# Performance work log

Measured on AMD Instinct MI355X. Metric: run time of the kernel, lower is better.

The kernel has to match this reference:

```python
import jax, jax.numpy as jnp
import numpy as np

N_TX, N_ACC, E = 500000, 100000, 1000000
D_TX, D_ACC, H = 64, 32, 64


def setup_inputs() -> dict:
    key = jax.random.key(0)
    ks = jax.random.split(key, 16)
    s = 0.05
    return {
        "x_tx": jax.random.normal(ks[0], (N_TX, D_TX), jnp.float32),
        "x_acc": jax.random.normal(ks[1], (N_ACC, D_ACC), jnp.float32),
        "pays_src": jax.random.randint(ks[2], (E,), 0, N_ACC),
        "pays_dst": jax.random.randint(ks[3], (E,), 0, N_TX),
        "rev_src": jax.random.randint(ks[4], (E,), 0, N_TX),
        "rev_dst": jax.random.randint(ks[5], (E,), 0, N_ACC),
        # SAGEConv for ('account','pays','transaction'): lin_l: D_ACC->H (bias), lin_r: D_TX->H (no bias)
        "Wl_pays": jax.random.normal(ks[6], (D_ACC, H), jnp.float32) * s,
        "bl_pays": jnp.zeros((H,), jnp.float32),
        "Wr_pays": jax.random.normal(ks[7], (D_TX, H), jnp.float32) * s,
        # SAGEConv for ('transaction','rev_pays','account'): lin_l: D_TX->H, lin_r: D_ACC->H
        "Wl_rev": jax.random.normal(ks[8], (D_TX, H), jnp.float32) * s,
        "bl_rev": jnp.zeros((H,), jnp.float32),
        "Wr_rev": jax.random.normal(ks[9], (D_ACC, H), jnp.float32) * s,
        # output head Linear(H, 1)
        "W_out": jax.random.normal(ks[10], (H, 1), jnp.float32) * s,
        "b_out": jnp.zeros((1,), jnp.float32),
    }


def _segment_mean(msg, dst, n_dst):
    # scatter-mean: sum per dst node / clamped degree (isolated nodes -> 0)
    s = jax.ops.segment_sum(msg, dst, num_segments=n_dst)
    c = jax.ops.segment_sum(jnp.ones((dst.shape[0], 1), msg.dtype), dst, num_segments=n_dst)
    return s / jnp.maximum(c, 1.0)


def _sage(x_src, x_dst, src, dst, Wl, bl, Wr):
    agg = _segment_mean(x_src[src], dst, x_dst.shape[0])  # [n_dst, d_src]
    return agg @ Wl + bl + x_dst @ Wr  # [n_dst, H]


def reference(x_tx, x_acc, pays_src, pays_dst, rev_src, rev_dst,
              Wl_pays, bl_pays, Wr_pays, Wl_rev, bl_rev, Wr_rev, W_out, b_out):
    # HeteroConv: each dst node type receives exactly one edge type here, so aggr='mean' is identity
    h_tx = _sage(x_acc, x_tx, pays_src, pays_dst, Wl_pays, bl_pays, Wr_pays)
    h_acc = _sage(x_tx, x_acc, rev_src, rev_dst, Wl_rev, bl_rev, Wr_rev)
    tx_x = jax.nn.relu(h_tx)
    _ = jax.nn.relu(h_acc)  # computed by the module but unused downstream
    logits = (tx_x @ W_out + b_out)[:, 0]
    return logits, tx_x
```

## Files before the change

### kernel.cpp

```cpp
#include <hip/hip_runtime.h>

#define N_TX   500000
#define N_ACC  100000
#define E_CNT  1000000
#define D_TX   64
#define D_ACC  32
#define H_DIM  64

#define SCAN_B    256
#define SCAN_I    8
#define SCAN_TILE (SCAN_B * SCAN_I)
#define NSCAN_BLOCKS ((N_TX + SCAN_TILE - 1) / SCAN_TILE)


__global__ __launch_bounds__(256) void hist_kernel(
    const int* __restrict__ dst, int* __restrict__ cnt) {
    int e = blockIdx.x * blockDim.x + threadIdx.x;
    if (e < E_CNT) atomicAdd(&cnt[dst[e]], 1);
}

__global__ __launch_bounds__(SCAN_B) void scan1_kernel(
    const int* __restrict__ cnt, int* __restrict__ offs, int* __restrict__ bsum) {
    __shared__ int lds[SCAN_B];
    int base = blockIdx.x * SCAN_TILE + threadIdx.x * SCAN_I;
    int v[SCAN_I];
    int tsum = 0;
#pragma unroll
    for (int i = 0; i < SCAN_I; ++i) {
        int idx = base + i;
        v[i] = (idx < N_TX) ? cnt[idx] : 0;
        tsum += v[i];
    }
    lds[threadIdx.x] = tsum;
    __syncthreads();
    for (int off = 1; off < SCAN_B; off <<= 1) {
        int a = 0;
        if ((int)threadIdx.x >= off) a = lds[threadIdx.x - off];
        __syncthreads();
        lds[threadIdx.x] += a;
        __syncthreads();
    }
    int texcl = lds[threadIdx.x] - tsum;
    if (threadIdx.x == SCAN_B - 1) bsum[blockIdx.x] = lds[SCAN_B - 1];
    int run = texcl;
#pragma unroll
    for (int i = 0; i < SCAN_I; ++i) {
        int idx = base + i;
        if (idx < N_TX) offs[idx] = run;
        run += v[i];
    }
}

__global__ __launch_bounds__(256) void scan2_kernel(int* __restrict__ bsum, int nb) {
    __shared__ int lds[256];
    int t = threadIdx.x;
    int v = (t < nb) ? bsum[t] : 0;
    lds[t] = v;
    __syncthreads();
    for (int off = 1; off < 256; off <<= 1) {
        int a = 0;
        if (t >= off) a = lds[t - off];
        __syncthreads();
        lds[t] += a;
        __syncthreads();
    }
    if (t < nb) bsum[t] = lds[t] - v;
}

__global__ __launch_bounds__(256) void finalize_kernel(
    int* __restrict__ offs, int* __restrict__ cursors, const int* __restrict__ bsum) {
    int i = blockIdx.x * blockDim.x + threadIdx.x;
    if (i < N_TX) {
        int f = offs[i] + bsum[i / SCAN_TILE];
        offs[i] = f;
        cursors[i] = f;
    }
}

__global__ __launch_bounds__(256) void fill_kernel(
    const int* __restrict__ src, const int* __restrict__ dst,
    int* __restrict__ cursors, int* __restrict__ eidx) {
    int e = blockIdx.x * blockDim.x + threadIdx.x;
    if (e < E_CNT) {
        int d = dst[e];
        int p = atomicAdd(&cursors[d], 1);
        eidx[p] = src[e];
    }
}

__global__ __launch_bounds__(256, 4) void acc_transform_kernel(
    const float* __restrict__ x_acc, const float* __restrict__ Wl,
    float* __restrict__ y, int rows_per_wave) {
    int lane = threadIdx.x & 63;
    int wave = (blockIdx.x * blockDim.x + threadIdx.x) >> 6;
    float wl[D_ACC];
#pragma unroll
    for (int k = 0; k < D_ACC; ++k) wl[k] = Wl[k * H_DIM + lane];
#pragma unroll
    for (int k = 0; k < D_ACC; ++k) asm volatile("" : "+v"(wl[k]));
    int r0 = wave * rows_per_wave;
    int r1 = min(r0 + rows_per_wave, N_ACC);
    for (int row = r0; row < r1; ++row) {
        int urow = __builtin_amdgcn_readfirstlane(row);
        const float4* xr = (const float4*)(x_acc + (size_t)urow * D_ACC);
        float a0 = 0.f, a1 = 0.f, a2 = 0.f, a3 = 0.f;
#pragma unroll
        for (int q = 0; q < 8; ++q) {
            float4 v = xr[q];
            a0 = fmaf(v.x, wl[4 * q + 0], a0);
            a1 = fmaf(v.y, wl[4 * q + 1], a1);
            a2 = fmaf(v.z, wl[4 * q + 2], a2);
            a3 = fmaf(v.w, wl[4 * q + 3], a3);
        }
        y[(size_t)urow * H_DIM + lane] = (a0 + a1) + (a2 + a3);
    }
}

__global__ __launch_bounds__(256, 4) void row_kernel(
    const float* __restrict__ x_tx,
    const float* __restrict__ y,
    const int*   __restrict__ offs,
    const int*   __restrict__ cnt,
    const int*   __restrict__ eidx,
    const float* __restrict__ Wr,
    const float* __restrict__ bl,
    const float* __restrict__ Wout,
    const float* __restrict__ bout,
    float*       __restrict__ logits,
    float*       __restrict__ txx) {
    int lane = threadIdx.x & 63;
    int wave = (blockIdx.x * blockDim.x + threadIdx.x) >> 6;

    int rbase = wave * 64;
    if (rbase >= N_TX) return;
    int nrows = min(64, N_TX - rbase);

    float wr[D_TX];
#pragma unroll
    for (int k = 0; k < D_TX; ++k) wr[k] = Wr[k * H_DIM + lane];
#pragma unroll
    for (int k = 0; k < D_TX; ++k) asm volatile("" : "+v"(wr[k]));
    float b  = bl[lane];
    float wo = Wout[lane];
    float bo = bout[0];
    asm volatile("" : "+v"(b), "+v"(wo), "+v"(bo));

    int deg_l = 0, off_l = 0;
    if (lane < nrows) {
        deg_l = cnt[rbase + lane];
        off_l = offs[rbase + lane];
    }
    int s0_l = 0, s1_l = 0, s2_l = 0, s3_l = 0;
    if (deg_l > 0) s0_l = eidx[off_l];
    if (deg_l > 1) s1_l = eidx[off_l + 1];
    if (deg_l > 2) s2_l = eidx[off_l + 2];
    if (deg_l > 3) s3_l = eidx[off_l + 3];

    int ubase = __builtin_amdgcn_readfirstlane(rbase);

    for (int k = 0; k < nrows; ++k) {
        int urow = ubase + k;
        int deg = __builtin_amdgcn_readlane(deg_l, k);
        int off = __builtin_amdgcn_readlane(off_l, k);
        int s0  = __builtin_amdgcn_readlane(s0_l, k);
        int s1  = __builtin_amdgcn_readlane(s1_l, k);
        int s2  = __builtin_amdgcn_readlane(s2_l, k);
        int s3  = __builtin_amdgcn_readlane(s3_l, k);

        float v0 = 0.f, v1 = 0.f, v2 = 0.f, v3 = 0.f;
        if (deg > 0) v0 = y[(size_t)s0 * H_DIM + lane];
        if (deg > 1) v1 = y[(size_t)s1 * H_DIM + lane];
        if (deg > 2) v2 = y[(size_t)s2 * H_DIM + lane];
        if (deg > 3) v3 = y[(size_t)s3 * H_DIM + lane];

        const float4* xr = (const float4*)(x_tx + (size_t)urow * D_TX);
        float a0 = 0.f, a1 = 0.f, a2 = 0.f, a3 = 0.f;
#pragma unroll
        for (int q = 0; q < 16; ++q) {
            float4 xv = xr[q];
            a0 = fmaf(xv.x, wr[4 * q + 0], a0);
            a1 = fmaf(xv.y, wr[4 * q + 1], a1);
            a2 = fmaf(xv.z, wr[4 * q + 2], a2);
            a3 = fmaf(xv.w, wr[4 * q + 3], a3);
        }

        float g = (v0 + v1) + (v2 + v3);
        for (int e = 4; e < deg; ++e) {
            int se = __builtin_amdgcn_readfirstlane(eidx[off + e]);
            g += y[(size_t)se * H_DIM + lane];
        }

        float inv = 1.0f / (float)(deg > 0 ? deg : 1);
        float h = ((a0 + a1) + (a2 + a3)) + b + g * inv;
        float r = fmaxf(h, 0.f);
        txx[(size_t)urow * H_DIM + lane] = r;

        float p = r * wo;
#pragma unroll
        for (int sh = 32; sh > 0; sh >>= 1) p += __shfl_down(p, sh);
        if (lane == 0) logits[urow] = p + bo;
    }
}

extern "C" void kernel_launch(void* const* d_in, const int* in_sizes, int n_in,
                              void* d_out, int out_size, void* d_ws, size_t ws_size,
                              hipStream_t stream) {
    const float* x_tx     = (const float*)d_in[0];
    const float* x_acc    = (const float*)d_in[1];
    const int*   pays_src = (const int*)d_in[2];
    const int*   pays_dst = (const int*)d_in[3];
    const float* Wl   = (const float*)d_in[6];
    const float* bl   = (const float*)d_in[7];
    const float* Wr   = (const float*)d_in[8];
    const float* Wout = (const float*)d_in[12];
    const float* bout = (const float*)d_in[13];

    float* out    = (float*)d_out;
    float* logits = out;
    float* txx    = out + N_TX;

    int* cnt     = (int*)d_ws;
    int* offs    = cnt + N_TX;
    int* cursors = offs + N_TX;
    int* bsum    = cursors + N_TX;
    int* eidx    = bsum + 1024;
    float* y     = (float*)(eidx + E_CNT);

    hipMemsetAsync(cnt, 0, (size_t)N_TX * sizeof(int), stream);

    hist_kernel<<<(E_CNT + 255) / 256, 256, 0, stream>>>(pays_dst, cnt);
    scan1_kernel<<<NSCAN_BLOCKS, SCAN_B, 0, stream>>>(cnt, offs, bsum);
    scan2_kernel<<<1, 256, 0, stream>>>(bsum, NSCAN_BLOCKS);
    finalize_kernel<<<(N_TX + 255) / 256, 256, 0, stream>>>(offs, cursors, bsum);
    fill_kernel<<<(E_CNT + 255) / 256, 256, 0, stream>>>(pays_src, pays_dst, cursors, eidx);

    {
        const int blocks = 2048;
        int rpw = (N_ACC + blocks * 4 - 1) / (blocks * 4);
        acc_transform_kernel<<<blocks, 256, 0, stream>>>(x_acc, Wl, y, rpw);
    }

    {
        const int waves  = (N_TX + 63) / 64;
        const int blocks = (waves + 3) / 4;
        row_kernel<<<blocks, 256, 0, stream>>>(
            x_tx, y, offs, cnt, eidx, Wr, bl, Wout, bout, logits, txx);
    }
}
```

Baseline: 628.2 us.

## Stage x_tx rows through double-buffered LDS with coalesced register prefetch

The row kernel now loads 16-row tiles of x_tx with coalesced float4 loads across the wave into registers, then stores them into a per-wave double-buffered LDS region. The next tile's global loads are issued before the current tile is computed, overlapping memory latency with the FMA work. The old code used wave-uniform scalar-address loads of each row straight from global memory. In exchange the kernel uses 32KB of LDS per block and more registers, which may lower occupancy. It also adds LDS read traffic in the inner loop.

```diff
diff --git a/kernel.cpp b/kernel.cpp
--- a/kernel.cpp
+++ b/kernel.cpp
@@ -11,6 +11,9 @@
 #define SCAN_I    8
 #define SCAN_TILE (SCAN_B * SCAN_I)
 #define NSCAN_BLOCKS ((N_TX + SCAN_TILE - 1) / SCAN_TILE)
+
+#define TROWS 16
+#define TFL4  (TROWS * H_DIM / 4)
 
 
 __global__ __launch_bounds__(256) void hist_kernel(
@@ -128,12 +131,18 @@
     const float* __restrict__ bout,
     float*       __restrict__ logits,
     float*       __restrict__ txx) {
+    __shared__ float xs[4 * 2 * TROWS * H_DIM];
+
     int lane = threadIdx.x & 63;
+    int wib  = threadIdx.x >> 6;
     int wave = (blockIdx.x * blockDim.x + threadIdx.x) >> 6;
 
     int rbase = wave * 64;
     if (rbase >= N_TX) return;
     int nrows = min(64, N_TX - rbase);
+
+    float* xbuf0 = xs + wib * (2 * TROWS * H_DIM);
+    float* xbuf1 = xbuf0 + TROWS * H_DIM;
 
     float wr[D_TX];
 #pragma unroll
@@ -157,48 +166,87 @@
     if (deg_l > 3) s3_l = eidx[off_l + 3];
 
     int ubase = __builtin_amdgcn_readfirstlane(rbase);
-
-    for (int k = 0; k < nrows; ++k) {
-        int urow = ubase + k;
-        int deg = __builtin_amdgcn_readlane(deg_l, k);
-        int off = __builtin_amdgcn_readlane(off_l, k);
-        int s0  = __builtin_amdgcn_readlane(s0_l, k);
-        int s1  = __builtin_amdgcn_readlane(s1_l, k);
-        int s2  = __builtin_amdgcn_readlane(s2_l, k);
-        int s3  = __builtin_amdgcn_readlane(s3_l, k);
-
-        float v0 = 0.f, v1 = 0.f, v2 = 0.f, v3 = 0.f;
-        if (deg > 0) v0 = y[(size_t)s0 * H_DIM + lane];
-        if (deg > 1) v1 = y[(size_t)s1 * H_DIM + lane];
-        if (deg > 2) v2 = y[(size_t)s2 * H_DIM + lane];
-        if (deg > 3) v3 = y[(size_t)s3 * H_DIM + lane];
-
-        const float4* xr = (const float4*)(x_tx + (size_t)urow * D_TX);
-        float a0 = 0.f, a1 = 0.f, a2 = 0.f, a3 = 0.f;
-#pragma unroll
-        for (int q = 0; q < 16; ++q) {
-            float4 xv = xr[q];
-            a0 = fmaf(xv.x, wr[4 * q + 0], a0);
-            a1 = fmaf(xv.y, wr[4 * q + 1], a1);
-            a2 = fmaf(xv.z, wr[4 * q + 2], a2);
-            a3 = fmaf(xv.w, wr[4 * q + 3], a3);
-        }
-
-        float g = (v0 + v1) + (v2 + v3);
-        for (int e = 4; e < deg; ++e) {
-            int se = __builtin_amdgcn_readfirstlane(eidx[off + e]);
-            g += y[(size_t)se * H_DIM + lane];
-        }
-
-        float inv = 1.0f / (float)(deg > 0 ? deg : 1);
-        float h = ((a0 + a1) + (a2 + a3)) + b + g * inv;
-        float r = fmaxf(h, 0.f);
-        txx[(size_t)urow * H_DIM + lane] = r;
-
-        float p = r * wo;
-#pragma unroll
-        for (int sh = 32; sh > 0; sh >>= 1) p += __shfl_down(p, sh);
-        if (lane == 0) logits[urow] = p + bo;
+    const float4* xsrc = (const float4*)(x_tx + (size_t)ubase * D_TX);
+
+    float4 st[4];
+#pragma unroll
+    for (int j = 0; j < 4; ++j) {
+        int f  = j * 64 + lane;
+        int gr = ubase + (f >> 4);
+        if (gr < N_TX) st[j] = xsrc[f];
+        else           st[j] = make_float4(0.f, 0.f, 0.f, 0.f);
+    }
+    {
+        float4* db = (float4*)xbuf0;
+#pragma unroll
+        for (int j = 0; j < 4; ++j) db[j * 64 + lane] = st[j];
+    }
+
+    for (int t = 0; t < 4; ++t) {
+        float* cur = (t & 1) ? xbuf1 : xbuf0;
+
+        if (t < 3) {
+#pragma unroll
+            for (int j = 0; j < 4; ++j) {
+                int f  = (t + 1) * TFL4 + j * 64 + lane;
+                int gr = ubase + (f >> 4);
+                if (gr < N_TX) st[j] = xsrc[f];
+                else           st[j] = make_float4(0.f, 0.f, 0.f, 0.f);
+            }
+        }
+
+        int kend = min(TROWS, nrows - t * TROWS);
+        for (int kk = 0; kk < kend; ++kk) {
+            int k   = t * TROWS + kk;
+            int urow = ubase + k;
+            int deg = __builtin_amdgcn_readlane(deg_l, k);
+            int off = __builtin_amdgcn_readlane(off_l, k);
+            int s0  = __builtin_amdgcn_readlane(s0_l, k);
+            int s1  = __builtin_amdgcn_readlane(s1_l, k);
+            int s2  = __builtin_amdgcn_readlane(s2_l, k);
+            int s3  = __builtin_amdgcn_readlane(s3_l, k);
+
+            float v0 = 0.f, v1 = 0.f, v2 = 0.f, v3 = 0.f;
+            if (deg > 0) v0 = y[(size_t)s0 * H_DIM + lane];
+            if (deg > 1) v1 = y[(size_t)s1 * H_DIM + lane];
+            if (deg > 2) v2 = y[(size_t)s2 * H_DIM + lane];
+            if (deg > 3) v3 = y[(size_t)s3 * H_DIM + lane];
+
+            const float4* xr = (const float4*)(cur + kk * H_DIM);
+            float a0 = 0.f, a1 = 0.f, a2 = 0.f, a3 = 0.f;
+#pragma unroll
+            for (int q = 0; q < 16; ++q) {
+                float4 xv = xr[q];
+                a0 = fmaf(xv.x, wr[4 * q + 0], a0);
+                a1 = fmaf(xv.y, wr[4 * q + 1], a1);
+                a2 = fmaf(xv.z, wr[4 * q + 2], a2);
+                a3 = fmaf(xv.w, wr[4 * q + 3], a3);
+            }
+
+            float g = (v0 + v1) + (v2 + v3);
+            for (int e = 4; e < deg; ++e) {
+                int se = __builtin_amdgcn_readfirstlane(eidx[off + e]);
+                g += y[(size_t)se * H_DIM + lane];
+            }
+
+            float inv = 1.0f / (float)(deg > 0 ? deg : 1);
+            float h = ((a0 + a1) + (a2 + a3)) + b + g * inv;
+            float r = fmaxf(h, 0.f);
+            txx[(size_t)urow * H_DIM + lane] = r;
+
+            float p = r * wo;
+#pragma unroll
+            for (int sh = 32; sh > 0; sh >>= 1) p += __shfl_down(p, sh);
+            if (lane == 0) logits[urow] = p + bo;
+        }
+
+        if (nrows <= (t + 1) * TROWS) break;
+
+        if (t < 3) {
+            float4* db = (float4*)((t & 1) ? xbuf0 : xbuf1);
+#pragma unroll
+            for (int j = 0; j < 4; ++j) db[j * 64 + lane] = st[j];
+        }
     }
 }
 
```

Result: slower. 2.035 ms (+223.9%).
